# Optimization experiments

Hardware: AMD Instinct MI355X
Metric: run time of the kernel (lower is better)

Reference implementation:

```python
import jax, jax.numpy as jnp
import numpy as np

N_NODES = 50000


def gcn_conv(h, W, b, src, dst, n_nodes):
    # PyG GCNConv: h' = D^{-1/2} (A + I) D^{-1/2} (h @ W) + b
    h = h @ W  # [N, out]
    deg = jax.ops.segment_sum(jnp.ones_like(dst, dtype=h.dtype), dst, num_segments=n_nodes)
    dinv = jnp.where(deg > 0, jax.lax.rsqrt(deg), 0.0)  # [N]
    norm = dinv[src] * dinv[dst]  # [E]
    msg = h[src] * norm[:, None]  # [E, out]
    out = jax.ops.segment_sum(msg, dst, num_segments=n_nodes)
    return out + b


def setup_inputs() -> dict:
    key = jax.random.key(0)
    ks = jax.random.split(key, 12)
    N, E, P, D, H = N_NODES, 1600000, 200000, 128, 128
    s = lambda fan_in: 1.0 / np.sqrt(fan_in)
    return {
        "x": jax.random.normal(ks[0], (N, D), dtype=jnp.float32),
        "edge_index": jax.random.randint(ks[1], (2, E), 0, N, dtype=jnp.int32),
        "drug_pairs": jax.random.randint(ks[2], (P, 2), 0, N, dtype=jnp.int32),
        "W1": jax.random.normal(ks[3], (D, H), dtype=jnp.float32) * s(D),
        "b1": jnp.zeros((H,), dtype=jnp.float32),
        "W2": jax.random.normal(ks[4], (H, H), dtype=jnp.float32) * s(H),
        "b2": jnp.zeros((H,), dtype=jnp.float32),
        "Wh1": jax.random.normal(ks[5], (2 * H, H), dtype=jnp.float32) * s(2 * H),
        "bh1": jnp.zeros((H,), dtype=jnp.float32),
        "Wh2": jax.random.normal(ks[6], (H, 1), dtype=jnp.float32) * s(H),
        "bh2": jnp.zeros((1,), dtype=jnp.float32),
    }


def reference(x, edge_index, drug_pairs, W1, b1, W2, b2, Wh1, bh1, Wh2, bh2):
    n = x.shape[0]
    # add self-loops once (GCNConv default add_self_loops=True)
    loop = jnp.arange(n, dtype=edge_index.dtype)
    src = jnp.concatenate([edge_index[0], loop])
    dst = jnp.concatenate([edge_index[1], loop])

    h = jax.nn.relu(gcn_conv(x, W1, b1, src, dst, n))  # dropout = identity (eval)
    h = jax.nn.relu(gcn_conv(h, W2, b2, src, dst, n))

    combined = jnp.concatenate([h[drug_pairs[:, 0]], h[drug_pairs[:, 1]]], axis=1)  # [P, 2H]
    out = jax.nn.relu(combined @ Wh1 + bh1) @ Wh2 + bh2  # [P, 1]
    return out
```

## Files before the change

kernel.cpp:

```cpp
#include <hip/hip_runtime.h>
#include <hip/hip_fp16.h>


#define BSH 9
#define BSZ (1 << BSH)
#define MSB 4096
#define XPAD 132
#define HB 256

typedef __attribute__((ext_vector_type(8))) short bf16x8;
typedef __attribute__((ext_vector_type(8))) _Float16 f16x8;
typedef __attribute__((ext_vector_type(4))) float f32x4;

__device__ __forceinline__ void acc8s(uint4 u, float f, float4& lo, float4& hi) {
  float2 f0 = __half22float2(((const __half2*)&u)[0]);
  float2 f1 = __half22float2(((const __half2*)&u)[1]);
  float2 f2 = __half22float2(((const __half2*)&u)[2]);
  float2 f3 = __half22float2(((const __half2*)&u)[3]);
  lo.x = fmaf(f, f0.x, lo.x); lo.y = fmaf(f, f0.y, lo.y);
  lo.z = fmaf(f, f1.x, lo.z); lo.w = fmaf(f, f1.y, lo.w);
  hi.x = fmaf(f, f2.x, hi.x); hi.y = fmaf(f, f2.y, hi.y);
  hi.z = fmaf(f, f3.x, hi.z); hi.w = fmaf(f, f3.y, hi.w);
}

__device__ __forceinline__ float4 h4_to_f4(uint2 u) {
  float2 fa = __half22float2(*(__half2*)&u.x);
  float2 fb = __half22float2(*(__half2*)&u.y);
  return make_float4(fa.x, fa.y, fb.x, fb.y);
}

__device__ __forceinline__ void split8(const float* v, bf16x8& hi, bf16x8& lo) {
#pragma unroll
  for (int j = 0; j < 8; ++j) {
    unsigned u = __float_as_uint(v[j]);
    hi[j] = (short)(u >> 16);
    float lf = v[j] - __uint_as_float(u & 0xffff0000u);
    lo[j] = (short)(__float_as_uint(lf) >> 16);
  }
}

__global__ __launch_bounds__(256) void k_prep_w(
    const float* __restrict__ W1, const float* __restrict__ W2,
    const float* __restrict__ Wh1, short* __restrict__ fragH,
    short* __restrict__ fragL, int* __restrict__ gcnt, int* __restrict__ gcur,
    int kb) {
  if (blockIdx.x == 32) {
    int t = threadIdx.x;
    if (t < kb) { gcnt[t] = 0; gcur[t] = 0; }
    return;
  }
  int g = blockIdx.x * 256 + threadIdx.x;
  int w = g >> 11;
  int rem = g & 2047;
  int lane = rem & 63;
  int ts = rem >> 6;
  int t = ts >> 2, s = ts & 3;
  int n = (t << 4) + (lane & 15);
  int k0 = s * 32 + (lane >> 4) * 8;
  const float* W = (w == 0) ? W1 : (w == 1) ? W2 : (w == 2) ? Wh1 : (Wh1 + 128 * 128);
  short h[8], l[8];
#pragma unroll
  for (int j = 0; j < 8; ++j) {
    float x = W[(k0 + j) * 128 + n];
    if (w == 0) {
      unsigned u = __float_as_uint(x);
      h[j] = (short)(u >> 16);
      float lf = x - __uint_as_float(u & 0xffff0000u);
      l[j] = (short)(__float_as_uint(lf) >> 16);
    } else {
      __half hh = __float2half(x);
      h[j] = __half_as_short(hh);
      l[j] = __half_as_short(__float2half(x - __half2float(hh)));
    }
  }
  ((int4*)fragH)[g] = *(int4*)h;
  ((int4*)fragL)[g] = *(int4*)l;
}

__device__ __forceinline__ void gemm1_body(
    const float* __restrict__ X, const short* __restrict__ fragH,
    const short* __restrict__ fragL, __half* __restrict__ C16, int n,
    int bid, float* sX) {
  int tid = threadIdx.x;
  int row0 = bid * 64;
  const float2* X2 = (const float2*)(X + (size_t)row0 * 128);
#pragma unroll
  for (int it = 0; it < 16; ++it) {
    int t = it * 256 + tid;
    int r = t >> 6, c2 = t & 63;
    int gr = row0 + r;
    float2 v = (gr < n) ? X2[t] : make_float2(0.f, 0.f);
    *(float2*)&sX[r * XPAD + c2 * 2] = v;
  }
  __syncthreads();
  int wid = tid >> 6, lane = tid & 63;
  int r0 = row0 + wid * 16;
  if (r0 >= n) return;
  int m = lane & 15, quad = lane >> 4;
  const float* xrow = sX + (wid * 16 + m) * XPAD;
  f32x4 acc[8];
#pragma unroll
  for (int t = 0; t < 8; ++t) acc[t] = (f32x4)(0.f);
  const int4* FH = (const int4*)fragH;
  const int4* FL = (const int4*)fragL;
#pragma unroll
  for (int s = 0; s < 4; ++s) {
    int k0 = s * 32 + quad * 8;
    float xv[8];
    *(float2*)&xv[0] = *(const float2*)(xrow + k0);
    *(float2*)&xv[2] = *(const float2*)(xrow + k0 + 2);
    *(float2*)&xv[4] = *(const float2*)(xrow + k0 + 4);
    *(float2*)&xv[6] = *(const float2*)(xrow + k0 + 6);
    bf16x8 ah, al;
    split8(xv, ah, al);
#pragma unroll
    for (int t = 0; t < 8; ++t) {
      int idx = (t * 4 + s) * 64 + lane;
      bf16x8 bh = *(const bf16x8*)&FH[idx];
      bf16x8 bl = *(const bf16x8*)&FL[idx];
      acc[t] = __builtin_amdgcn_mfma_f32_16x16x32_bf16(ah, bh, acc[t], 0, 0, 0);
      acc[t] = __builtin_amdgcn_mfma_f32_16x16x32_bf16(al, bh, acc[t], 0, 0, 0);
      acc[t] = __builtin_amdgcn_mfma_f32_16x16x32_bf16(ah, bl, acc[t], 0, 0, 0);
    }
  }
#pragma unroll
  for (int t = 0; t < 8; ++t) {
#pragma unroll
    for (int r = 0; r < 4; ++r) {
      int row = r0 + quad * 4 + r;
      C16[(size_t)row * 128 + t * 16 + m] = __float2half(acc[t][r]);
    }
  }
}

__global__ __launch_bounds__(256) void k_gemm_hist(
    const float* __restrict__ X, const short* __restrict__ fragH,
    const short* __restrict__ fragL, __half* __restrict__ C16, int n, int gb,
    const int* __restrict__ dst, int* __restrict__ gcnt, int e, int kb) {
  __shared__ float sX[64 * XPAD];
  if ((int)blockIdx.x < gb) {
    gemm1_body(X, fragH, fragL, C16, n, blockIdx.x, sX);
    return;
  }
  int bid = blockIdx.x - gb;
  int* h4 = (int*)sX;
  int tid = threadIdx.x, wid = tid >> 6;
  for (int t = tid; t < 512; t += 256) h4[t] = 0;
  __syncthreads();
  for (int i = bid * 256 + tid; i < e; i += HB * 256) {
    int d = __builtin_nontemporal_load(&dst[i]);
    atomicAdd(&h4[wid * 128 + (d >> BSH)], 1);
  }
  __syncthreads();
  if (tid < kb)
    atomicAdd(&gcnt[tid], h4[tid] + h4[128 + tid] + h4[256 + tid] + h4[384 + tid]);
}

__global__ __launch_bounds__(256) void k_gemm_f16(
    const __half* __restrict__ X16, const short* __restrict__ fragH,
    const short* __restrict__ fragL, const float* __restrict__ rowscale,
    __half* __restrict__ C16, int n) {
  int wid = threadIdx.x >> 6, lane = threadIdx.x & 63;
  int r0 = (blockIdx.x * 4 + wid) * 16;
  if (r0 >= n) return;
  int m = lane & 15, quad = lane >> 4;
  const uint4* Xr = (const uint4*)(X16 + (size_t)(r0 + m) * 128);
  f32x4 acc[8];
#pragma unroll
  for (int t = 0; t < 8; ++t) acc[t] = (f32x4)(0.f);
  const int4* FH = (const int4*)fragH;
  const int4* FL = (const int4*)fragL;
#pragma unroll
  for (int s = 0; s < 4; ++s) {
    uint4 av = Xr[quad + 4 * s];
    f16x8 a = *(const f16x8*)&av;
#pragma unroll
    for (int t = 0; t < 8; ++t) {
      int idx = (t * 4 + s) * 64 + lane;
      int4 bhv = FH[idx], blv = FL[idx];
      f16x8 bh = *(const f16x8*)&bhv;
      f16x8 bl = *(const f16x8*)&blv;
      acc[t] = __builtin_amdgcn_mfma_f32_16x16x32_f16(a, bh, acc[t], 0, 0, 0);
      acc[t] = __builtin_amdgcn_mfma_f32_16x16x32_f16(a, bl, acc[t], 0, 0, 0);
    }
  }
  float sc[4];
#pragma unroll
  for (int r = 0; r < 4; ++r)
    sc[r] = rowscale ? rowscale[r0 + quad * 4 + r] : 1.f;
#pragma unroll
  for (int t = 0; t < 8; ++t) {
#pragma unroll
    for (int r = 0; r < 4; ++r) {
      int row = r0 + quad * 4 + r;
      C16[(size_t)row * 128 + t * 16 + m] = __float2half(acc[t][r] * sc[r]);
    }
  }
}

__global__ __launch_bounds__(256) void k_gemm_dual_f16(
    const __half* __restrict__ X16,
    const short* __restrict__ fHa, const short* __restrict__ fLa,
    const short* __restrict__ fHb, const short* __restrict__ fLb,
    __half* __restrict__ A16, __half* __restrict__ B16, int n) {
  int wid = threadIdx.x >> 6, lane = threadIdx.x & 63;
  int r0 = (blockIdx.x * 4 + wid) * 16;
  if (r0 >= n) return;
  int m = lane & 15, quad = lane >> 4;
  const uint4* Xr = (const uint4*)(X16 + (size_t)(r0 + m) * 128);
  f32x4 accA[8], accB[8];
#pragma unroll
  for (int t = 0; t < 8; ++t) { accA[t] = (f32x4)(0.f); accB[t] = (f32x4)(0.f); }
  const int4* FHa = (const int4*)fHa; const int4* FLa = (const int4*)fLa;
  const int4* FHb = (const int4*)fHb; const int4* FLb = (const int4*)fLb;
#pragma unroll
  for (int s = 0; s < 4; ++s) {
    uint4 av = Xr[quad + 4 * s];
    f16x8 a = *(const f16x8*)&av;
#pragma unroll
    for (int t = 0; t < 8; ++t) {
      int idx = (t * 4 + s) * 64 + lane;
      int4 v0 = FHa[idx], v1 = FLa[idx], v2 = FHb[idx], v3 = FLb[idx];
      accA[t] = __builtin_amdgcn_mfma_f32_16x16x32_f16(a, *(const f16x8*)&v0, accA[t], 0, 0, 0);
      accA[t] = __builtin_amdgcn_mfma_f32_16x16x32_f16(a, *(const f16x8*)&v1, accA[t], 0, 0, 0);
      accB[t] = __builtin_amdgcn_mfma_f32_16x16x32_f16(a, *(const f16x8*)&v2, accB[t], 0, 0, 0);
      accB[t] = __builtin_amdgcn_mfma_f32_16x16x32_f16(a, *(const f16x8*)&v3, accB[t], 0, 0, 0);
    }
  }
#pragma unroll
  for (int t = 0; t < 8; ++t) {
#pragma unroll
    for (int r = 0; r < 4; ++r) {
      int row = r0 + quad * 4 + r;
      A16[(size_t)row * 128 + t * 16 + m] = __float2half(accA[t][r]);
      B16[(size_t)row * 128 + t * 16 + m] = __float2half(accB[t][r]);
    }
  }
}

__global__ __launch_bounds__(256) void k_multisplit(const int* __restrict__ src,
                                                    const int* __restrict__ dst,
                                                    const int* __restrict__ gcnt,
                                                    int* __restrict__ gcur,
                                                    int* __restrict__ tmp,
                                                    int e, int kb) {
  __shared__ int h4[4 * 128], off[4 * 128], sbase[128], ws[2];
  int tid = threadIdx.x, wid = tid >> 6, lane = tid & 63;
  for (int t = tid; t < 512; t += 256) h4[t] = 0;
  __syncthreads();
  int i0 = blockIdx.x * MSB + tid;
  int d[16], rk[16];
#pragma unroll
  for (int u = 0; u < 16; ++u) {
    int i = i0 + u * 256;
    if (i < e) {
      d[u] = __builtin_nontemporal_load(&dst[i]);
      rk[u] = atomicAdd(&h4[wid * 128 + (d[u] >> BSH)], 1);
    }
  }
  __syncthreads();
  int tot = 0;
  if (tid < 128) {
    int c0 = h4[tid], c1 = h4[128 + tid], c2 = h4[256 + tid], c3 = h4[384 + tid];
    off[tid] = 0; off[128 + tid] = c0;
    off[256 + tid] = c0 + c1; off[384 + tid] = c0 + c1 + c2;
    tot = c0 + c1 + c2 + c3;
  }
  int v = (tid < 128 && tid < kb) ? gcnt[tid] : 0;
  int orig = v;
#pragma unroll
  for (int o = 1; o < 64; o <<= 1) {
    int u = __shfl_up(v, o, 64);
    if (lane >= o) v += u;
  }
  if (lane == 63 && wid < 2) ws[wid] = v;
  __syncthreads();
  if (tid < 128) sbase[tid] = ((wid == 1) ? ws[0] : 0) + v - orig;
  __syncthreads();
  if (tid < kb && tot > 0) sbase[tid] += atomicAdd(&gcur[tid], tot);
  __syncthreads();
#pragma unroll
  for (int u = 0; u < 16; ++u) {
    int i = i0 + u * 256;
    if (i < e) {
      int s = __builtin_nontemporal_load(&src[i]);
      int k = d[u] >> BSH;
      tmp[sbase[k] + off[wid * 128 + k] + rk[u]] = ((d[u] & (BSZ - 1)) << 16) | s;
    }
  }
}

__global__ __launch_bounds__(512) void k_bucket_build(
    const int* __restrict__ tmp, const int* __restrict__ gcnt,
    int* __restrict__ rowptr, float* __restrict__ dinv,
    unsigned short* __restrict__ colarr, int n, int kb, int e) {
  __shared__ int dl[BSZ], cl[BSZ], sbase[128], ws[8];
  int t = threadIdx.x, b = blockIdx.x;
  int lane = t & 63, w = t >> 6;
  int v = (t < 128 && t < kb) ? gcnt[t] : 0;
  int orig0 = v;
#pragma unroll
  for (int o = 1; o < 64; o <<= 1) {
    int u = __shfl_up(v, o, 64);
    if (lane >= o) v += u;
  }
  if (lane == 63 && w < 2) ws[w] = v;
  dl[t] = 0;
  __syncthreads();
  if (t < 128) sbase[t] = ((w == 1) ? ws[0] : 0) + v - orig0;
  __syncthreads();
  int s0 = sbase[b];
  int s1 = s0 + gcnt[b];
  for (int j = s0 + t; j < s1; j += 512)
    atomicAdd(&dl[((unsigned)tmp[j]) >> 16], 1);
  __syncthreads();
  int dv = dl[t], orig = dv;
#pragma unroll
  for (int o = 1; o < 64; o <<= 1) {
    int u = __shfl_up(dv, o, 64);
    if (lane >= o) dv += u;
  }
  if (lane == 63) ws[w] = dv;
  __syncthreads();
  if (t == 0) {
    int a = 0;
#pragma unroll
    for (int k = 0; k < 8; ++k) { int x = ws[k]; ws[k] = a; a += x; }
  }
  __syncthreads();
  int ex = ws[w] + dv - orig;
  cl[t] = ex;
  int node = (b << BSH) + t;
  if (node < n) {
    rowptr[node] = s0 + ex;
    dinv[node] = rsqrtf((float)(orig + 1));
  }
  if (b == kb - 1 && t == 0) rowptr[n] = e;
  __syncthreads();
  for (int j = s0 + t; j < s1; j += 512) {
    int p = tmp[j];
    int r = atomicAdd(&cl[((unsigned)p) >> 16], 1);
    colarr[s0 + r] = (unsigned short)(p & 0xFFFF);
  }
}

__global__ __launch_bounds__(256) void k_agg_h(
    const __half2* __restrict__ g2, const float* __restrict__ dinv,
    const float* __restrict__ srcscale,
    const int* __restrict__ rowptr, const unsigned short* __restrict__ col,
    const float* __restrict__ bias, __half* __restrict__ out16, int n) {
  int i = blockIdx.x * 4 + (threadIdx.x >> 6);
  if (i >= n) return;
  int lane = threadIdx.x & 63;
  int sub = lane >> 4;
  int c8 = lane & 15;
  const uint4* G = (const uint4*)g2;
  float di = dinv[i];
  float4 z = make_float4(0.f, 0.f, 0.f, 0.f);
  float4 lo0 = z, lo1 = z, lo2 = z, lo3 = z, hi0 = z, hi1 = z, hi2 = z, hi3 = z;
  if (sub == 0)
    acc8s(G[(size_t)i * 16 + c8], srcscale ? di : 1.f, lo0, hi0);
  int beg = rowptr[i], end = rowptr[i + 1];
  int j = beg;
  for (; j + 16 <= end; j += 16) {
    int s0 = __builtin_nontemporal_load(&col[j + sub]);
    int s1 = __builtin_nontemporal_load(&col[j + 4 + sub]);
    int s2 = __builtin_nontemporal_load(&col[j + 8 + sub]);
    int s3 = __builtin_nontemporal_load(&col[j + 12 + sub]);
    float f0 = srcscale ? srcscale[s0] : 1.f;
    float f1 = srcscale ? srcscale[s1] : 1.f;
    float f2 = srcscale ? srcscale[s2] : 1.f;
    float f3 = srcscale ? srcscale[s3] : 1.f;
    uint4 u0 = G[(size_t)s0 * 16 + c8];
    uint4 u1 = G[(size_t)s1 * 16 + c8];
    uint4 u2 = G[(size_t)s2 * 16 + c8];
    uint4 u3 = G[(size_t)s3 * 16 + c8];
    acc8s(u0, f0, lo0, hi0); acc8s(u1, f1, lo1, hi1);
    acc8s(u2, f2, lo2, hi2); acc8s(u3, f3, lo3, hi3);
  }
  for (; j + 4 <= end; j += 4) {
    int s0 = __builtin_nontemporal_load(&col[j + sub]);
    float f0 = srcscale ? srcscale[s0] : 1.f;
    acc8s(G[(size_t)s0 * 16 + c8], f0, lo1, hi1);
  }
  int rem = end - j;
  if (sub < rem) {
    int s0 = __builtin_nontemporal_load(&col[j + sub]);
    float f0 = srcscale ? srcscale[s0] : 1.f;
    acc8s(G[(size_t)s0 * 16 + c8], f0, lo2, hi2);
  }
  float4 lo, hi;
  lo.x = (lo0.x + lo1.x) + (lo2.x + lo3.x);
  lo.y = (lo0.y + lo1.y) + (lo2.y + lo3.y);
  lo.z = (lo0.z + lo1.z) + (lo2.z + lo3.z);
  lo.w = (lo0.w + lo1.w) + (lo2.w + lo3.w);
  hi.x = (hi0.x + hi1.x) + (hi2.x + hi3.x);
  hi.y = (hi0.y + hi1.y) + (hi2.y + hi3.y);
  hi.z = (hi0.z + hi1.z) + (hi2.z + hi3.z);
  hi.w = (hi0.w + hi1.w) + (hi2.w + hi3.w);
  lo.x += __shfl_down(lo.x, 32, 64); lo.x += __shfl_down(lo.x, 16, 64);
  lo.y += __shfl_down(lo.y, 32, 64); lo.y += __shfl_down(lo.y, 16, 64);
  lo.z += __shfl_down(lo.z, 32, 64); lo.z += __shfl_down(lo.z, 16, 64);
  lo.w += __shfl_down(lo.w, 32, 64); lo.w += __shfl_down(lo.w, 16, 64);
  hi.x += __shfl_down(hi.x, 32, 64); hi.x += __shfl_down(hi.x, 16, 64);
  hi.y += __shfl_down(hi.y, 32, 64); hi.y += __shfl_down(hi.y, 16, 64);
  hi.z += __shfl_down(hi.z, 32, 64); hi.z += __shfl_down(hi.z, 16, 64);
  hi.w += __shfl_down(hi.w, 32, 64); hi.w += __shfl_down(hi.w, 16, 64);
  if (sub == 0) {
    float4 b0 = ((const float4*)bias)[2 * c8];
    float4 b1 = ((const float4*)bias)[2 * c8 + 1];
    __half2 q0 = __floats2half2_rn(fmaxf(fmaf(di, lo.x, b0.x), 0.f),
                                   fmaxf(fmaf(di, lo.y, b0.y), 0.f));
    __half2 q1 = __floats2half2_rn(fmaxf(fmaf(di, lo.z, b0.z), 0.f),
                                   fmaxf(fmaf(di, lo.w, b0.w), 0.f));
    __half2 q2 = __floats2half2_rn(fmaxf(fmaf(di, hi.x, b1.x), 0.f),
                                   fmaxf(fmaf(di, hi.y, b1.y), 0.f));
    __half2 q3 = __floats2half2_rn(fmaxf(fmaf(di, hi.z, b1.z), 0.f),
                                   fmaxf(fmaf(di, hi.w, b1.w), 0.f));
    uint4 o;
    o.x = *(unsigned*)&q0; o.y = *(unsigned*)&q1;
    o.z = *(unsigned*)&q2; o.w = *(unsigned*)&q3;
    ((uint4*)out16)[(size_t)i * 16 + c8] = o;
  }
}

__global__ __launch_bounds__(256) void k_pairs_h(
    const __half2* __restrict__ A, const __half2* __restrict__ B,
    const int* __restrict__ pairs, const float* __restrict__ bh1,
    const float* __restrict__ wh2, const float* __restrict__ bh2,
    float* __restrict__ out, int P) {
  int p = blockIdx.x * 4 + (threadIdx.x >> 6);
  int lane = threadIdx.x & 63;
  if (p >= P) return;
  int sub = lane >> 5, c4 = lane & 31;
  int p0 = pairs[2 * p], p1 = pairs[2 * p + 1];
  const uint2* T4 = sub ? (const uint2*)B : (const uint2*)A;
  int row = sub ? p1 : p0;
  float4 v = h4_to_f4(T4[(size_t)row * 32 + c4]);
  v.x += __shfl_xor(v.x, 32, 64);
  v.y += __shfl_xor(v.y, 32, 64);
  v.z += __shfl_xor(v.z, 32, 64);
  v.w += __shfl_xor(v.w, 32, 64);
  float4 bi = ((const float4*)bh1)[c4];
  float4 wv = ((const float4*)wh2)[c4];
  float s = fmaxf(v.x + bi.x, 0.f) * wv.x + fmaxf(v.y + bi.y, 0.f) * wv.y +
            fmaxf(v.z + bi.z, 0.f) * wv.z + fmaxf(v.w + bi.w, 0.f) * wv.w;
#pragma unroll
  for (int o = 16; o > 0; o >>= 1) s += __shfl_down(s, o, 64);
  if (lane == 0) out[p] = s + bh2[0];
}

extern "C" void kernel_launch(void* const* d_in, const int* in_sizes, int n_in,
                              void* d_out, int out_size, void* d_ws, size_t ws_size,
                              hipStream_t stream) {
  const float* x   = (const float*)d_in[0];
  const int* ei    = (const int*)d_in[1];
  const int* pairs = (const int*)d_in[2];
  const float* W1  = (const float*)d_in[3];
  const float* b1  = (const float*)d_in[4];
  const float* W2  = (const float*)d_in[5];
  const float* b2  = (const float*)d_in[6];
  const float* Wh1 = (const float*)d_in[7];
  const float* bh1 = (const float*)d_in[8];
  const float* Wh2 = (const float*)d_in[9];
  const float* bh2 = (const float*)d_in[10];
  (void)n_in; (void)out_size; (void)ws_size;

  int N = in_sizes[0] / 128;
  int E = in_sizes[1] / 2;
  int P = in_sizes[2] / 2;
  const int* src = ei;
  const int* dst = ei + E;
  int KB = (N + BSZ - 1) >> BSH;

  char* wsp = (char*)d_ws;
  size_t off = 0;
  auto alloc = [&](size_t bytes) -> void* {
    void* p = wsp + off;
    off += (bytes + 255) & ~(size_t)255;
    return p;
  };
  __half* g16 = (__half*)alloc((size_t)N * 128 * 2);
  __half* h1  = (__half*)alloc((size_t)N * 128 * 2);
  __half* h2  = (__half*)alloc((size_t)N * 128 * 2);
  float* dinv = (float*)alloc((size_t)N * 4);
  int* rowptr = (int*)alloc((size_t)(N + 1) * 4);
  unsigned short* colarr = (unsigned short*)alloc((size_t)E * 2);
  int* tmp    = (int*)alloc((size_t)E * 4);
  short* fragH = (short*)alloc(4 * 2048 * 8 * 2);
  short* fragL = (short*)alloc(4 * 2048 * 8 * 2);
  int* gcnt  = (int*)alloc((size_t)(KB + 1) * 4);
  int* gcur  = (int*)alloc((size_t)(KB + 1) * 4);
  __half* A16 = g16;
  __half* B16 = h1;
  short* fH_W1 = fragH + 0 * 16384;  short* fL_W1 = fragL + 0 * 16384;
  short* fH_W2 = fragH + 1 * 16384;  short* fL_W2 = fragL + 1 * 16384;
  short* fH_Wa = fragH + 2 * 16384;  short* fL_Wa = fragL + 2 * 16384;
  short* fH_Wb = fragH + 3 * 16384;  short* fL_Wb = fragL + 3 * 16384;

  int GB = (N + 63) / 64;
  int GF = (N / 16 + 3) / 4;
  int AB = (N + 3) / 4;

  k_prep_w<<<33, 256, 0, stream>>>(W1, W2, Wh1, fragH, fragL, gcnt, gcur, KB);
  k_gemm_hist<<<GB + HB, 256, 0, stream>>>(x, fH_W1, fL_W1, g16, N, GB,
                                           dst, gcnt, E, KB);
  k_multisplit<<<(E + MSB - 1) / MSB, 256, 0, stream>>>(src, dst, gcnt, gcur,
                                                        tmp, E, KB);
  k_bucket_build<<<KB, 512, 0, stream>>>(tmp, gcnt, rowptr, dinv, colarr, N, KB, E);
  k_agg_h<<<AB, 256, 0, stream>>>((const __half2*)g16, dinv, dinv, rowptr,
                                  colarr, b1, h1, N);
  k_gemm_f16<<<GF, 256, 0, stream>>>(h1, fH_W2, fL_W2, dinv, g16, N);
  k_agg_h<<<AB, 256, 0, stream>>>((const __half2*)g16, dinv, nullptr, rowptr,
                                  colarr, b2, h2, N);
  k_gemm_dual_f16<<<GF, 256, 0, stream>>>(h2, fH_Wa, fL_Wa, fH_Wb, fL_Wb,
                                          A16, B16, N);
  k_pairs_h<<<(P + 3) / 4, 256, 0, stream>>>((const __half2*)A16, (const __half2*)B16,
                                             pairs, bh1, Wh2, bh2, (float*)d_out, P);
}
```

Baseline: 394.9 us.

## Fold source dinv scaling into first GEMM epilogue, move histogram to prep kernel

The first GEMM now runs after the bucket build, so it can multiply each output row by dinv in its epilogue. This removes the per-edge srcscale gather and FMA from the first aggregation, which now does plain fp16 adds. To make that ordering possible, the edge histogram moves into the weight-prep kernel and the counter zeroing becomes memsets. The cost is that GEMM1 can no longer overlap with the histogram and instead sits on the critical path after the CSR build, with one extra launch.

Measured after the change: 370.9 us. 6.1% less time.

```diff
diff --git a/kernel.cpp b/kernel.cpp
--- a/kernel.cpp
+++ b/kernel.cpp
@@ -12,15 +12,13 @@
 typedef __attribute__((ext_vector_type(8))) _Float16 f16x8;
 typedef __attribute__((ext_vector_type(4))) float f32x4;
 
-__device__ __forceinline__ void acc8s(uint4 u, float f, float4& lo, float4& hi) {
+__device__ __forceinline__ void acc8(uint4 u, float4& lo, float4& hi) {
   float2 f0 = __half22float2(((const __half2*)&u)[0]);
   float2 f1 = __half22float2(((const __half2*)&u)[1]);
   float2 f2 = __half22float2(((const __half2*)&u)[2]);
   float2 f3 = __half22float2(((const __half2*)&u)[3]);
-  lo.x = fmaf(f, f0.x, lo.x); lo.y = fmaf(f, f0.y, lo.y);
-  lo.z = fmaf(f, f1.x, lo.z); lo.w = fmaf(f, f1.y, lo.w);
-  hi.x = fmaf(f, f2.x, hi.x); hi.y = fmaf(f, f2.y, hi.y);
-  hi.z = fmaf(f, f3.x, hi.z); hi.w = fmaf(f, f3.y, hi.w);
+  lo.x += f0.x; lo.y += f0.y; lo.z += f1.x; lo.w += f1.y;
+  hi.x += f2.x; hi.y += f2.y; hi.z += f3.x; hi.w += f3.y;
 }
 
 __device__ __forceinline__ float4 h4_to_f4(uint2 u) {
@@ -39,14 +37,24 @@
   }
 }
 
-__global__ __launch_bounds__(256) void k_prep_w(
+__global__ __launch_bounds__(256) void k_prep_hist(
     const float* __restrict__ W1, const float* __restrict__ W2,
     const float* __restrict__ Wh1, short* __restrict__ fragH,
-    short* __restrict__ fragL, int* __restrict__ gcnt, int* __restrict__ gcur,
-    int kb) {
-  if (blockIdx.x == 32) {
-    int t = threadIdx.x;
-    if (t < kb) { gcnt[t] = 0; gcur[t] = 0; }
+    short* __restrict__ fragL,
+    const int* __restrict__ dst, int* __restrict__ gcnt, int e, int kb) {
+  if (blockIdx.x >= 32) {
+    __shared__ int h4[512];
+    int bid = blockIdx.x - 32;
+    int tid = threadIdx.x, wid = tid >> 6;
+    for (int t = tid; t < 512; t += 256) h4[t] = 0;
+    __syncthreads();
+    for (int i = bid * 256 + tid; i < e; i += HB * 256) {
+      int d = __builtin_nontemporal_load(&dst[i]);
+      atomicAdd(&h4[wid * 128 + (d >> BSH)], 1);
+    }
+    __syncthreads();
+    if (tid < kb)
+      atomicAdd(&gcnt[tid], h4[tid] + h4[128 + tid] + h4[256 + tid] + h4[384 + tid]);
     return;
   }
   int g = blockIdx.x * 256 + threadIdx.x;
@@ -77,12 +85,13 @@
   ((int4*)fragL)[g] = *(int4*)l;
 }
 
-__device__ __forceinline__ void gemm1_body(
+__global__ __launch_bounds__(256) void k_gemm_mfma(
     const float* __restrict__ X, const short* __restrict__ fragH,
-    const short* __restrict__ fragL, __half* __restrict__ C16, int n,
-    int bid, float* sX) {
+    const short* __restrict__ fragL, const float* __restrict__ rowscale,
+    __half* __restrict__ C16, int n) {
+  __shared__ float sX[64 * XPAD];
   int tid = threadIdx.x;
-  int row0 = bid * 64;
+  int row0 = blockIdx.x * 64;
   const float2* X2 = (const float2*)(X + (size_t)row0 * 128);
 #pragma unroll
   for (int it = 0; it < 16; ++it) {
@@ -123,37 +132,18 @@
       acc[t] = __builtin_amdgcn_mfma_f32_16x16x32_bf16(ah, bl, acc[t], 0, 0, 0);
     }
   }
+  float sc[4];
+#pragma unroll
+  for (int r = 0; r < 4; ++r)
+    sc[r] = rowscale[r0 + quad * 4 + r];
 #pragma unroll
   for (int t = 0; t < 8; ++t) {
 #pragma unroll
     for (int r = 0; r < 4; ++r) {
       int row = r0 + quad * 4 + r;
-      C16[(size_t)row * 128 + t * 16 + m] = __float2half(acc[t][r]);
-    }
-  }
-}
-
-__global__ __launch_bounds__(256) void k_gemm_hist(
-    const float* __restrict__ X, const short* __restrict__ fragH,
-    const short* __restrict__ fragL, __half* __restrict__ C16, int n, int gb,
-    const int* __restrict__ dst, int* __restrict__ gcnt, int e, int kb) {
-  __shared__ float sX[64 * XPAD];
-  if ((int)blockIdx.x < gb) {
-    gemm1_body(X, fragH, fragL, C16, n, blockIdx.x, sX);
-    return;
-  }
-  int bid = blockIdx.x - gb;
-  int* h4 = (int*)sX;
-  int tid = threadIdx.x, wid = tid >> 6;
-  for (int t = tid; t < 512; t += 256) h4[t] = 0;
-  __syncthreads();
-  for (int i = bid * 256 + tid; i < e; i += HB * 256) {
-    int d = __builtin_nontemporal_load(&dst[i]);
-    atomicAdd(&h4[wid * 128 + (d >> BSH)], 1);
-  }
-  __syncthreads();
-  if (tid < kb)
-    atomicAdd(&gcnt[tid], h4[tid] + h4[128 + tid] + h4[256 + tid] + h4[384 + tid]);
+      C16[(size_t)row * 128 + t * 16 + m] = __float2half(acc[t][r] * sc[r]);
+    }
+  }
 }
 
 __global__ __launch_bounds__(256) void k_gemm_f16(
@@ -346,7 +336,6 @@
 
 __global__ __launch_bounds__(256) void k_agg_h(
     const __half2* __restrict__ g2, const float* __restrict__ dinv,
-    const float* __restrict__ srcscale,
     const int* __restrict__ rowptr, const unsigned short* __restrict__ col,
     const float* __restrict__ bias, __half* __restrict__ out16, int n) {
   int i = blockIdx.x * 4 + (threadIdx.x >> 6);
@@ -355,11 +344,9 @@
   int sub = lane >> 4;
   int c8 = lane & 15;
   const uint4* G = (const uint4*)g2;
-  float di = dinv[i];
   float4 z = make_float4(0.f, 0.f, 0.f, 0.f);
   float4 lo0 = z, lo1 = z, lo2 = z, lo3 = z, hi0 = z, hi1 = z, hi2 = z, hi3 = z;
-  if (sub == 0)
-    acc8s(G[(size_t)i * 16 + c8], srcscale ? di : 1.f, lo0, hi0);
+  if (sub == 0) acc8(G[(size_t)i * 16 + c8], lo0, hi0);
   int beg = rowptr[i], end = rowptr[i + 1];
   int j = beg;
   for (; j + 16 <= end; j += 16) {
@@ -367,27 +354,21 @@
     int s1 = __builtin_nontemporal_load(&col[j + 4 + sub]);
     int s2 = __builtin_nontemporal_load(&col[j + 8 + sub]);
     int s3 = __builtin_nontemporal_load(&col[j + 12 + sub]);
-    float f0 = srcscale ? srcscale[s0] : 1.f;
-    float f1 = srcscale ? srcscale[s1] : 1.f;
-    float f2 = srcscale ? srcscale[s2] : 1.f;
-    float f3 = srcscale ? srcscale[s3] : 1.f;
     uint4 u0 = G[(size_t)s0 * 16 + c8];
     uint4 u1 = G[(size_t)s1 * 16 + c8];
     uint4 u2 = G[(size_t)s2 * 16 + c8];
     uint4 u3 = G[(size_t)s3 * 16 + c8];
-    acc8s(u0, f0, lo0, hi0); acc8s(u1, f1, lo1, hi1);
-    acc8s(u2, f2, lo2, hi2); acc8s(u3, f3, lo3, hi3);
+    acc8(u0, lo0, hi0); acc8(u1, lo1, hi1);
+    acc8(u2, lo2, hi2); acc8(u3, lo3, hi3);
   }
   for (; j + 4 <= end; j += 4) {
     int s0 = __builtin_nontemporal_load(&col[j + sub]);
-    float f0 = srcscale ? srcscale[s0] : 1.f;
-    acc8s(G[(size_t)s0 * 16 + c8], f0, lo1, hi1);
+    acc8(G[(size_t)s0 * 16 + c8], lo1, hi1);
   }
   int rem = end - j;
   if (sub < rem) {
     int s0 = __builtin_nontemporal_load(&col[j + sub]);
-    float f0 = srcscale ? srcscale[s0] : 1.f;
-    acc8s(G[(size_t)s0 * 16 + c8], f0, lo2, hi2);
+    acc8(G[(size_t)s0 * 16 + c8], lo2, hi2);
   }
   float4 lo, hi;
   lo.x = (lo0.x + lo1.x) + (lo2.x + lo3.x);
@@ -407,6 +388,7 @@
   hi.z += __shfl_down(hi.z, 32, 64); hi.z += __shfl_down(hi.z, 16, 64);
   hi.w += __shfl_down(hi.w, 32, 64); hi.w += __shfl_down(hi.w, 16, 64);
   if (sub == 0) {
+    float di = dinv[i];
     float4 b0 = ((const float4*)bias)[2 * c8];
     float4 b1 = ((const float4*)bias)[2 * c8 + 1];
     __half2 q0 = __floats2half2_rn(fmaxf(fmaf(di, lo.x, b0.x), 0.f),
@@ -502,17 +484,17 @@
   int GF = (N / 16 + 3) / 4;
   int AB = (N + 3) / 4;
 
-  k_prep_w<<<33, 256, 0, stream>>>(W1, W2, Wh1, fragH, fragL, gcnt, gcur, KB);
-  k_gemm_hist<<<GB + HB, 256, 0, stream>>>(x, fH_W1, fL_W1, g16, N, GB,
+  hipMemsetAsync(gcnt, 0, (size_t)(KB + 1) * 4, stream);
+  hipMemsetAsync(gcur, 0, (size_t)(KB + 1) * 4, stream);
+  k_prep_hist<<<32 + HB, 256, 0, stream>>>(W1, W2, Wh1, fragH, fragL,
                                            dst, gcnt, E, KB);
   k_multisplit<<<(E + MSB - 1) / MSB, 256, 0, stream>>>(src, dst, gcnt, gcur,
                                                         tmp, E, KB);
   k_bucket_build<<<KB, 512, 0, stream>>>(tmp, gcnt, rowptr, dinv, colarr, N, KB, E);
-  k_agg_h<<<AB, 256, 0, stream>>>((const __half2*)g16, dinv, dinv, rowptr,
-                                  colarr, b1, h1, N);
+  k_gemm_mfma<<<GB, 256, 0, stream>>>(x, fH_W1, fL_W1, dinv, g16, N);
+  k_agg_h<<<AB, 256, 0, stream>>>((const __half2*)g16, dinv, rowptr, colarr, b1, h1, N);
   k_gemm_f16<<<GF, 256, 0, stream>>>(h1, fH_W2, fL_W2, dinv, g16, N);
-  k_agg_h<<<AB, 256, 0, stream>>>((const __half2*)g16, dinv, nullptr, rowptr,
-                                  colarr, b2, h2, N);
+  k_agg_h<<<AB, 256, 0, stream>>>((const __half2*)g16, dinv, rowptr, colarr, b2, h2, N);
   k_gemm_dual_f16<<<GF, 256, 0, stream>>>(h2, fH_Wa, fL_Wa, fH_Wb, fL_Wb,
                                           A16, B16, N);
   k_pairs_h<<<(P + 3) / 4, 256, 0, stream>>>((const __half2*)A16, (const __half2*)B16,
```
